# Performance work log

Measured on AMD Instinct MI355X. Metric: run time of the kernel, lower is better.

## Reference

```python
import jax, jax.numpy as jnp
import numpy as np

B, F, V, D = 4096, 8, 1000, 1024  # batch, n_fields, vocab per field, hidden_size
LN_EPS = 1e-5


def layer_norm(x, g, b, eps=LN_EPS):
    mu = x.mean(axis=-1, keepdims=True)
    var = ((x - mu) ** 2).mean(axis=-1, keepdims=True)
    return (x - mu) * jax.lax.rsqrt(var + eps) * g + b


def setup_inputs() -> dict:
    key = jax.random.key(0)
    k0, k1, k2, k3 = jax.random.split(key, 4)
    return {
        "input_embedding": jax.random.normal(k0, (B, D), jnp.float32),
        "features": jax.random.randint(k1, (B, F), 0, V),
        "embed_tables": jax.random.normal(k2, (F, V, D), jnp.float32) * 0.02,
        "ln_gamma": jnp.ones((D,), jnp.float32),
        "ln_beta": jnp.zeros((D,), jnp.float32),
        "pred_W": jax.random.normal(k3, (F, D, V), jnpp := jnp.float32) * 0.02,
        "pred_b": jnp.zeros((F, V), jnp.float32),
    }


def reference(input_embedding, features, embed_tables, ln_gamma, ln_beta, pred_W, pred_b):
    # Per-field embedding lookup: (B, F, D)
    feat_emb = embed_tables[jnp.arange(F)[None, :], features]
    # Stack input embedding first, as in torch.stack([input_embedding] + ...):
    embeddings = jnp.concatenate([input_embedding[:, None, :], feat_emb], axis=1)  # (B, F+1, D)
    # triu(diagonal=1) masked broadcast-sum then [:, 1:, :] == exclusive causal prefix sum:
    # masked_sums[:, j] = sum_{i < j+1} embeddings[:, i] for j = 0..F-1
    masked_sums = jnp.cumsum(embeddings, axis=1)[:, :F, :]  # (B, F, D)
    h = jax.nn.gelu(layer_norm(masked_sums, ln_gamma, ln_beta), approximate=False)
    # Per-field predictor heads (Linear(D, V)), batched over fields:
    logits = jnp.einsum("bfd,fdv->bfv", h, pred_W) + pred_b  # (B, F, V)
    return logits
```

## Files before the change

### kernel.cpp

```cpp
#include <hip/hip_runtime.h>
#include <hip/hip_bf16.h>

#define B_ 4096
#define F_ 8
#define V_ 1000
#define D_ 1024
#define VP 1024

typedef __bf16 bf16x8 __attribute__((ext_vector_type(8)));
typedef float f32x4 __attribute__((ext_vector_type(4)));

__device__ __forceinline__ void gload_lds16(const void* g, void* l) {
  __builtin_amdgcn_global_load_lds(
      (const __attribute__((address_space(1))) void*)g,
      (__attribute__((address_space(3))) void*)l, 16, 0, 0);
}

__global__ __launch_bounds__(256) void transpose_w(
    const float* __restrict__ W, __hip_bfloat16* __restrict__ Wt) {
  __shared__ float tile[32][33];
  const int f = blockIdx.z;
  const int k0 = blockIdx.x * 32;
  const int v0 = blockIdx.y * 32;
  const int tx = threadIdx.x;
  const int ty = threadIdx.y;
  const float* Wf = W + (size_t)f * D_ * V_;
#pragma unroll
  for (int i = 0; i < 4; ++i) {
    int k = k0 + ty + i * 8;
    int v = v0 + tx;
    tile[ty + i * 8][tx] = (v < V_) ? Wf[k * V_ + v] : 0.0f;
  }
  __syncthreads();
  __hip_bfloat16* Wtf = Wt + (size_t)f * VP * D_;
#pragma unroll
  for (int i = 0; i < 4; ++i) {
    int v = v0 + ty + i * 8;
    int k = k0 + tx;
    Wtf[v * D_ + k] = __float2bfloat16(tile[tx][ty + i * 8]);
  }
}

__global__ __launch_bounds__(256) void fuse_h(
    const float* __restrict__ emb, const int* __restrict__ feats,
    const float* __restrict__ tables, const float* __restrict__ gamma,
    const float* __restrict__ beta, __hip_bfloat16* __restrict__ H) {
  const int b = blockIdx.x;
  const int t = threadIdx.x;
  const int d = t * 4;
  const int wave = t >> 6, lane = t & 63;

  float s[4];
  {
    float4 v = *reinterpret_cast<const float4*>(&emb[(size_t)b * D_ + d]);
    s[0] = v.x; s[1] = v.y; s[2] = v.z; s[3] = v.w;
  }
  float gm[4], bt[4];
  {
    float4 g = *reinterpret_cast<const float4*>(&gamma[d]);
    float4 bb = *reinterpret_cast<const float4*>(&beta[d]);
    gm[0] = g.x; gm[1] = g.y; gm[2] = g.z; gm[3] = g.w;
    bt[0] = bb.x; bt[1] = bb.y; bt[2] = bb.z; bt[3] = bb.w;
  }
  __shared__ float red[2][4][2];

  for (int f = 0; f < F_; ++f) {
    float sum = s[0] + s[1] + s[2] + s[3];
    float ssq = s[0] * s[0] + s[1] * s[1] + s[2] * s[2] + s[3] * s[3];
#pragma unroll
    for (int off = 32; off > 0; off >>= 1) {
      sum += __shfl_xor(sum, off, 64);
      ssq += __shfl_xor(ssq, off, 64);
    }
    const int pb = f & 1;
    if (lane == 0) { red[pb][wave][0] = sum; red[pb][wave][1] = ssq; }
    __syncthreads();
    sum = red[pb][0][0] + red[pb][1][0] + red[pb][2][0] + red[pb][3][0];
    ssq = red[pb][0][1] + red[pb][1][1] + red[pb][2][1] + red[pb][3][1];

    const float mu = sum * (1.0f / D_);
    const float var = ssq * (1.0f / D_) - mu * mu;
    const float rstd = rsqrtf(var + 1e-5f);

    __hip_bfloat16 hb[4];
#pragma unroll
    for (int j = 0; j < 4; ++j) {
      float x = (s[j] - mu) * rstd * gm[j] + bt[j];
      float g = 0.5f * x * (1.0f + erff(x * 0.70710678118654752f));
      hb[j] = __float2bfloat16(g);
    }
    *reinterpret_cast<uint2*>(&H[(size_t)f * (B_ * D_) + (size_t)b * D_ + d]) =
        *reinterpret_cast<const uint2*>(hb);

    if (f < F_ - 1) {
      int feat = feats[b * F_ + f];
      const float* row = tables + ((size_t)f * V_ + feat) * D_;
      float4 tv = *reinterpret_cast<const float4*>(&row[d]);
      s[0] += tv.x; s[1] += tv.y; s[2] += tv.z; s[3] += tv.w;
    }
  }
}

#define AOFF 0
#define BOFF 32768

#define STAGE(OPB, GB, DBUF, HALF, KT)                                        \
  do {                                                                        \
    const ushort* _g = (GB) + (size_t)(HALF) * (128 * D_) + (size_t)(KT) * 64;\
    ushort* _l = &lds[(OPB) + ((DBUF)*2 + (HALF)) * 8192 + w * 512];          \
    gload_lds16(_g, _l);                                                      \
    gload_lds16(_g + 64 * D_, _l + 4096);                                     \
  } while (0)

#define LD_A(DST, LBASE, FIOFF)                                               \
  _Pragma("unroll") for (int _fj = 0; _fj < 4; ++_fj)                         \
  _Pragma("unroll") for (int _ks = 0; _ks < 2; ++_ks)                         \
      DST[_fj][_ks] = *reinterpret_cast<const bf16x8*>(                       \
          (LBASE) + ((((FIOFF) + _fj) * 2 + _ks) * 512));

#define LD_B(DST, LBASE, NFOFF)                                               \
  _Pragma("unroll") for (int _fn = 0; _fn < 2; ++_fn)                         \
  _Pragma("unroll") for (int _ks = 0; _ks < 2; ++_ks)                         \
      DST[_fn][_ks] = *reinterpret_cast<const bf16x8*>(                       \
          (LBASE) + ((((NFOFF) + _fn) * 2 + _ks) * 512));

#define Q_MFMA(AF, BF, R0, C0)                                                \
  do {                                                                        \
    __builtin_amdgcn_s_setprio(1);                                            \
    _Pragma("unroll") for (int _fj = 0; _fj < 4; ++_fj)                       \
    _Pragma("unroll") for (int _fn = 0; _fn < 2; ++_fn)                       \
    _Pragma("unroll") for (int _ks = 0; _ks < 2; ++_ks)                       \
        acc[(R0) + _fj][(C0) + _fn] =                                         \
            __builtin_amdgcn_mfma_f32_16x16x32_bf16(                          \
                AF[_fj][_ks], BF[_fn][_ks], acc[(R0) + _fj][(C0) + _fn],      \
                0, 0, 0);                                                     \
    __builtin_amdgcn_s_setprio(0);                                            \
  } while (0)

#define BAR __builtin_amdgcn_s_barrier()
#define SB0 __builtin_amdgcn_sched_barrier(0)
#define VM4 asm volatile("s_waitcnt vmcnt(4)")
#define VM0 asm volatile("s_waitcnt vmcnt(0)")
#define LG0 asm volatile("s_waitcnt lgkmcnt(0)")

__global__ __launch_bounds__(512, 2) void gemm_hw(
    const ushort* __restrict__ H,
    const ushort* __restrict__ Wt,
    const float* __restrict__ bias,
    float* __restrict__ out) {
  __shared__ ushort lds[65536];

  const int bid = blockIdx.x;
  const int swz = (bid & 7) * 64 + (bid >> 3);
  const int f = swz >> 6;
  const int r = swz & 63;
  const int mt = r >> 2, nt = r & 3;

  const int t = threadIdx.x;
  const int w = t >> 6, l = t & 63;
  const int wm = w >> 2;
  const int wn = w & 3;

  const ushort* Hf = H + (size_t)f * (B_ * D_);
  const ushort* Wf = Wt + (size_t)f * (VP * D_);

  const int srow = ((w >> 1) << 4) + (l >> 2);
  const int skx = ((w & 1) << 5) + ((((l & 3) << 3)) ^ (((l >> 5) & 1) << 4));
  const ushort* gA = Hf + (size_t)(mt * 256 + srow) * D_ + skx;
  const ushort* gB = Wf + (size_t)(nt * 256 + srow) * D_ + skx;

  const int laneu =
      ((l & 15) << 5) + (((((l >> 4) << 4)) ^ (((l >> 3) & 1) << 5)) >> 1);
  const ushort* lA[2] = {&lds[(0 * 2 + wm) * 8192 + laneu],
                         &lds[(1 * 2 + wm) * 8192 + laneu]};
  const ushort* lB[2] = {
      &lds[BOFF + (0 * 2 + (wn >> 1)) * 8192 + (wn & 1) * 4096 + laneu],
      &lds[BOFF + (1 * 2 + (wn >> 1)) * 8192 + (wn & 1) * 4096 + laneu]};

  bf16x8 a0[4][2], a1[4][2], b0[2][2], b1[2][2];
  f32x4 acc[8][4] = {};

  STAGE(AOFF, gA, 0, 0, 0);
  STAGE(AOFF, gA, 0, 1, 0);
  STAGE(BOFF, gB, 0, 0, 0);
  STAGE(BOFF, gB, 0, 1, 0);
  STAGE(AOFF, gA, 1, 0, 1);
  STAGE(AOFF, gA, 1, 1, 1);
  VM4;
  BAR;

#pragma unroll 1
  for (int i = 0; i < 8; ++i) {
    const int t1 = 2 * i + 1, t2 = 2 * i + 2, t3 = 2 * i + 3;
    const bool more = (i < 7);
    LD_A(a0, lA[0], 0);
    LD_B(b0, lB[0], 0);
    STAGE(BOFF, gB, 1, 0, t1);
    BAR;
    LG0;
    SB0;
    Q_MFMA(a0, b0, 0, 0);
    LD_A(a1, lA[0], 4);
    STAGE(BOFF, gB, 1, 1, t1);
    BAR;
    LG0;
    SB0;
    Q_MFMA(a1, b0, 4, 0);
    LD_B(b1, lB[0], 2);
    if (more) STAGE(AOFF, gA, 0, 0, t2);
    BAR;
    LG0;
    SB0;
    Q_MFMA(a0, b1, 0, 2);
    if (more) {
      STAGE(AOFF, gA, 0, 1, t2);
      VM4;
    } else {
      VM0;
    }
    BAR;
    SB0;
    Q_MFMA(a1, b1, 4, 2);
    LD_A(a0, lA[1], 0);
    LD_B(b0, lB[1], 0);
    if (more) STAGE(BOFF, gB, 0, 0, t2);
    BAR;
    LG0;
    SB0;
    Q_MFMA(a0, b0, 0, 0);
    LD_A(a1, lA[1], 4);
    if (more) STAGE(BOFF, gB, 0, 1, t2);
    BAR;
    LG0;
    SB0;
    Q_MFMA(a1, b0, 4, 0);
    LD_B(b1, lB[1], 2);
    if (more) STAGE(AOFF, gA, 1, 0, t3);
    BAR;
    LG0;
    SB0;
    Q_MFMA(a0, b1, 0, 2);
    if (more) {
      STAGE(AOFF, gA, 1, 1, t3);
      VM4;
    }
    BAR;
    SB0;
    Q_MFMA(a1, b1, 4, 2);
  }

  const float* bp = bias + f * V_;
  const int orow0 = mt * 256 + wm * 128 + ((l >> 4) << 2);
  const int ocol0 = nt * 256 + wn * 64 + (l & 15);
#pragma unroll
  for (int fi = 0; fi < 8; ++fi) {
#pragma unroll
    for (int fn = 0; fn < 4; ++fn) {
      int col = ocol0 + fn * 16;
      if (col < V_) {
        float bb = bp[col];
        int row = orow0 + fi * 16;
        float* op = out + (size_t)row * (F_ * V_) + (size_t)f * V_ + col;
#pragma unroll
        for (int q = 0; q < 4; ++q)
          op[(size_t)q * (F_ * V_)] = acc[fi][fn][q] + bb;
      }
    }
  }
}

extern "C" void kernel_launch(void* const* d_in, const int* in_sizes, int n_in,
                              void* d_out, int out_size, void* d_ws,
                              size_t ws_size, hipStream_t stream) {
  const float* emb = (const float*)d_in[0];
  const int* feats = (const int*)d_in[1];
  const float* tables = (const float*)d_in[2];
  const float* gamma = (const float*)d_in[3];
  const float* beta = (const float*)d_in[4];
  const float* W = (const float*)d_in[5];
  const float* bias = (const float*)d_in[6];
  float* out = (float*)d_out;

  char* ws = (char*)d_ws;
  __hip_bfloat16* Hbuf = (__hip_bfloat16*)ws;
  __hip_bfloat16* Wtbuf =
      (__hip_bfloat16*)(ws + (size_t)F_ * B_ * D_ * 2);

  transpose_w<<<dim3(D_ / 32, VP / 32, F_), dim3(32, 8), 0, stream>>>(W, Wtbuf);
  fuse_h<<<dim3(B_), dim3(256), 0, stream>>>(emb, feats, tables, gamma, beta,
                                             Hbuf);
  gemm_hw<<<dim3((B_ / 256) * (VP / 256) * F_), dim3(512), 0, stream>>>(
      (const ushort*)Hbuf, (const ushort*)Wtbuf, bias, out);
}
```

Baseline: 134.5 us.

## Software-pipeline LDS fragment reads with inline ds_read and partial lgkmcnt waits

Replaces the compiler-generated LDS fragment loads in the GEMM main loop with inline-asm ds_read_b128 using fixed immediate offsets. Fragments for the next MFMA quadrant are now read before the current quadrant's MFMAs run, and the full lgkmcnt(0) waits become partial lgkmcnt(N) waits so LDS reads overlap with matrix math. The quadrant order and the MFMA loop order (k-step outermost) are also rearranged. In exchange the schedule depends on hand-counted waitcnt values and assumes the shared array starts at LDS address zero, which makes it fragile and adds some risk of ordering mistakes.

```diff
diff --git a/kernel.cpp b/kernel.cpp
--- a/kernel.cpp
+++ b/kernel.cpp
@@ -112,36 +112,34 @@
     gload_lds16(_g + 64 * D_, _l + 4096);                                     \
   } while (0)
 
-#define LD_A(DST, LBASE, FIOFF)                                               \
-  _Pragma("unroll") for (int _fj = 0; _fj < 4; ++_fj)                         \
-  _Pragma("unroll") for (int _ks = 0; _ks < 2; ++_ks)                         \
-      DST[_fj][_ks] = *reinterpret_cast<const bf16x8*>(                       \
-          (LBASE) + ((((FIOFF) + _fj) * 2 + _ks) * 512));
-
-#define LD_B(DST, LBASE, NFOFF)                                               \
-  _Pragma("unroll") for (int _fn = 0; _fn < 2; ++_fn)                         \
-  _Pragma("unroll") for (int _ks = 0; _ks < 2; ++_ks)                         \
-      DST[_fn][_ks] = *reinterpret_cast<const bf16x8*>(                       \
-          (LBASE) + ((((NFOFF) + _fn) * 2 + _ks) * 512));
-
-#define Q_MFMA(AF, BF, R0, C0)                                                \
+#define DSR(D, BASE, O)                                                       \
+  asm volatile("ds_read_b128 %0, %1 offset:" O : "=v"(D) : "v"(BASE))
+
+#define RD4(ARR, I0, BASE, O0, O1, O2, O3)                                    \
+  do {                                                                        \
+    DSR(ARR[(I0) + 0], BASE, O0);                                             \
+    DSR(ARR[(I0) + 1], BASE, O1);                                             \
+    DSR(ARR[(I0) + 2], BASE, O2);                                             \
+    DSR(ARR[(I0) + 3], BASE, O3);                                             \
+  } while (0)
+
+#define QMF(AF, BF, R0, C0)                                                   \
   do {                                                                        \
     __builtin_amdgcn_s_setprio(1);                                            \
+    _Pragma("unroll") for (int _ks = 0; _ks < 2; ++_ks)                       \
     _Pragma("unroll") for (int _fj = 0; _fj < 4; ++_fj)                       \
     _Pragma("unroll") for (int _fn = 0; _fn < 2; ++_fn)                       \
-    _Pragma("unroll") for (int _ks = 0; _ks < 2; ++_ks)                       \
         acc[(R0) + _fj][(C0) + _fn] =                                         \
             __builtin_amdgcn_mfma_f32_16x16x32_bf16(                          \
-                AF[_fj][_ks], BF[_fn][_ks], acc[(R0) + _fj][(C0) + _fn],      \
-                0, 0, 0);                                                     \
+                AF[_fj * 2 + _ks], BF[_fn * 2 + _ks],                         \
+                acc[(R0) + _fj][(C0) + _fn], 0, 0, 0);                        \
     __builtin_amdgcn_s_setprio(0);                                            \
   } while (0)
 
 #define BAR __builtin_amdgcn_s_barrier()
 #define SB0 __builtin_amdgcn_sched_barrier(0)
 #define VM4 asm volatile("s_waitcnt vmcnt(4)")
-#define VM0 asm volatile("s_waitcnt vmcnt(0)")
-#define LG0 asm volatile("s_waitcnt lgkmcnt(0)")
+#define LGK(N) asm volatile("s_waitcnt lgkmcnt(" #N ")")
 
 __global__ __launch_bounds__(512, 2) void gemm_hw(
     const ushort* __restrict__ H,
@@ -171,13 +169,13 @@
 
   const int laneu =
       ((l & 15) << 5) + (((((l >> 4) << 4)) ^ (((l >> 3) & 1) << 5)) >> 1);
-  const ushort* lA[2] = {&lds[(0 * 2 + wm) * 8192 + laneu],
-                         &lds[(1 * 2 + wm) * 8192 + laneu]};
-  const ushort* lB[2] = {
-      &lds[BOFF + (0 * 2 + (wn >> 1)) * 8192 + (wn & 1) * 4096 + laneu],
-      &lds[BOFF + (1 * 2 + (wn >> 1)) * 8192 + (wn & 1) * 4096 + laneu]};
-
-  bf16x8 a0[4][2], a1[4][2], b0[2][2], b1[2][2];
+  const unsigned vA0 = (unsigned)(wm * 8192 + laneu) * 2u;
+  const unsigned vA1 = vA0 + 32768u;
+  const unsigned vB0 =
+      (unsigned)(32768 + (wn >> 1) * 8192 + (wn & 1) * 4096 + laneu) * 2u;
+  const unsigned vB1 = vB0 + 32768u;
+
+  bf16x8 a0[8], a1[8], b0f[4], b1f[4];
   f32x4 acc[8][4] = {};
 
   STAGE(AOFF, gA, 0, 0, 0);
@@ -188,65 +186,91 @@
   STAGE(AOFF, gA, 1, 1, 1);
   VM4;
   BAR;
+  RD4(a0, 0, vA0, "0", "1024", "2048", "3072");
+  RD4(a0, 4, vA0, "4096", "5120", "6144", "7168");
+  RD4(b0f, 0, vB0, "0", "1024", "2048", "3072");
+  SB0;
 
 #pragma unroll 1
   for (int i = 0; i < 8; ++i) {
     const int t1 = 2 * i + 1, t2 = 2 * i + 2, t3 = 2 * i + 3;
     const bool more = (i < 7);
-    LD_A(a0, lA[0], 0);
-    LD_B(b0, lB[0], 0);
+    BAR;
+    RD4(b1f, 0, vB0, "4096", "5120", "6144", "7168");
     STAGE(BOFF, gB, 1, 0, t1);
-    BAR;
-    LG0;
-    SB0;
-    Q_MFMA(a0, b0, 0, 0);
-    LD_A(a1, lA[0], 4);
+    LGK(4);
+    SB0;
+    QMF(a0, b0f, 0, 0);
+    SB0;
+    VM4;
+    BAR;
+    RD4(a1, 0, vA0, "8192", "9216", "10240", "11264");
+    RD4(a1, 4, vA0, "12288", "13312", "14336", "15360");
     STAGE(BOFF, gB, 1, 1, t1);
-    BAR;
-    LG0;
-    SB0;
-    Q_MFMA(a1, b0, 4, 0);
-    LD_B(b1, lB[0], 2);
+    LGK(8);
+    SB0;
+    QMF(a0, b1f, 0, 2);
+    SB0;
+    VM4;
+    BAR;
+    RD4(a0, 0, vA1, "0", "1024", "2048", "3072");
     if (more) STAGE(AOFF, gA, 0, 0, t2);
-    BAR;
-    LG0;
-    SB0;
-    Q_MFMA(a0, b1, 0, 2);
+    LGK(4);
+    SB0;
+    QMF(a1, b0f, 4, 0);
+    SB0;
+    VM4;
+    BAR;
+    RD4(a0, 4, vA1, "4096", "5120", "6144", "7168");
+    RD4(b0f, 0, vB1, "0", "1024", "2048", "3072");
+    if (more) STAGE(AOFF, gA, 0, 1, t2);
+    LGK(12);
+    SB0;
+    QMF(a1, b1f, 4, 2);
+    SB0;
+    VM4;
+    BAR;
+    RD4(b1f, 0, vB1, "4096", "5120", "6144", "7168");
+    RD4(a1, 0, vA1, "8192", "9216", "10240", "11264");
+    if (more) STAGE(BOFF, gB, 0, 0, t2);
+    LGK(8);
+    SB0;
+    QMF(a0, b0f, 0, 0);
+    SB0;
+    VM4;
+    BAR;
+    RD4(a1, 4, vA1, "12288", "13312", "14336", "15360");
+    if (more) STAGE(BOFF, gB, 0, 1, t2);
+    LGK(8);
+    SB0;
+    QMF(a0, b1f, 0, 2);
+    SB0;
+    VM4;
+    BAR;
     if (more) {
-      STAGE(AOFF, gA, 0, 1, t2);
-      VM4;
+      RD4(a0, 0, vA0, "0", "1024", "2048", "3072");
+      RD4(a0, 4, vA0, "4096", "5120", "6144", "7168");
+      STAGE(AOFF, gA, 1, 0, t3);
+      LGK(8);
     } else {
-      VM0;
-    }
-    BAR;
-    SB0;
-    Q_MFMA(a1, b1, 4, 2);
-    LD_A(a0, lA[1], 0);
-    LD_B(b0, lB[1], 0);
-    if (more) STAGE(BOFF, gB, 0, 0, t2);
-    BAR;
-    LG0;
-    SB0;
-    Q_MFMA(a0, b0, 0, 0);
-    LD_A(a1, lA[1], 4);
-    if (more) STAGE(BOFF, gB, 0, 1, t2);
-    BAR;
-    LG0;
-    SB0;
-    Q_MFMA(a1, b0, 4, 0);
-    LD_B(b1, lB[1], 2);
-    if (more) STAGE(AOFF, gA, 1, 0, t3);
-    BAR;
-    LG0;
-    SB0;
-    Q_MFMA(a0, b1, 0, 2);
+      LGK(0);
+    }
+    SB0;
+    QMF(a1, b0f, 4, 0);
+    SB0;
+    VM4;
+    BAR;
     if (more) {
+      RD4(b0f, 0, vB0, "0", "1024", "2048", "3072");
       STAGE(AOFF, gA, 1, 1, t3);
-      VM4;
-    }
-    BAR;
-    SB0;
-    Q_MFMA(a1, b1, 4, 2);
+      LGK(12);
+    } else {
+      LGK(0);
+    }
+    SB0;
+    QMF(a1, b1f, 4, 2);
+    SB0;
+    VM4;
   }
 
   const float* bp = bias + f * V_;
```

Measured after the change: 186.3 us. 38.5% more time.
